# Kernel tuning notes

Measured on AMD Instinct MI355X. Metric: run time of the kernel, lower is better.

Reference implementation:

```python
import jax, jax.numpy as jnp
import numpy as np

B, M, N = 32, 16, 256        # problems, constraints, items
P = M * N                    # nodes per problem graph (4096)
NODES = B * P                # 131072
E = 2_097_152                # edges (avg degree 16)
F_IN = 16
H = 128                      # n_hidden[0..5], n_hidden[7]
H6 = 256                     # n_hidden[6]


def setup_inputs() -> dict:
    key = jax.random.key(0)
    ks = jax.random.split(key, 24)
    nrm = lambda k, shape: jax.random.normal(k, shape, jnp.float32) * 0.05
    inp = {}
    inp["G"] = jax.random.normal(ks[0], (NODES, F_IN), jnp.float32)
    inp["edge_index"] = jax.random.randint(ks[1], (2, E), 0, NODES)
    inp["edge_weight"] = jax.random.uniform(ks[2], (E,), jnp.float32)
    inp["edge_attribute"] = jax.random.normal(ks[3], (E, 1), jnp.float32)  # unused, kept for API parity
    inp["value_var_solutions"] = jax.random.randint(ks[4], (B, P), 0, 2).astype(jnp.int32)
    inp["item_values"] = jax.random.uniform(ks[5], (B, N), jnp.float32)
    # learned parameters
    inp["W_emb1"], inp["b_emb1"] = nrm(ks[6], (F_IN, H)), jnp.zeros((H,), jnp.float32)
    inp["W_emb2"], inp["b_emb2"] = nrm(ks[7], (H, H)), jnp.zeros((H,), jnp.float32)
    for i, t in enumerate(("c1", "c2")):  # GatedGraphConv(H, num_layers=2) x2
        inp[f"{t}_W"]  = nrm(ks[8 + 3 * i], (2, H, H))
        inp[f"{t}_wi"] = nrm(ks[9 + 3 * i], (3 * H, H))
        inp[f"{t}_wh"] = nrm(ks[10 + 3 * i], (3 * H, H))
        inp[f"{t}_bi"] = jnp.zeros((3 * H,), jnp.float32)
        inp[f"{t}_bh"] = jnp.zeros((3 * H,), jnp.float32)
    inp["W_g1"], inp["b_g1"] = nrm(ks[14], (H, H)), jnp.zeros((H,), jnp.float32)
    inp["W_g2"], inp["b_g2"] = nrm(ks[15], (H, H)), jnp.zeros((H,), jnp.float32)
    inp["W_l1"], inp["b_l1"] = nrm(ks[16], (2 * H, H6)), jnp.zeros((H6,), jnp.float32)
    inp["W_l2"], inp["b_l2"] = nrm(ks[17], (H6, H)), jnp.zeros((H,), jnp.float32)
    inp["W_l3"], inp["b_l3"] = nrm(ks[18], (H, 1)), jnp.zeros((1,), jnp.float32)
    return inp


def _gru_cell(m, h, wi, wh, bi, bh):
    # torch.nn.GRUCell with gate order (r, z, n)
    gi = m @ wi.T + bi
    gh = h @ wh.T + bh
    ir, iz, inn = jnp.split(gi, 3, axis=-1)
    hr, hz, hn = jnp.split(gh, 3, axis=-1)
    r = jax.nn.sigmoid(ir + hr)
    z = jax.nn.sigmoid(iz + hz)
    n = jnp.tanh(inn + r * hn)
    return (1.0 - z) * n + z * h


def _gated_graph_conv(x, src, dst, ew, W, wi, wh, bi, bh):
    # PyG GatedGraphConv: for each layer, m_i = sum_{j->i} ew * (x_j @ W_l); x = GRU(m, x)
    nnodes = x.shape[0]
    for l in range(W.shape[0]):
        msg = (x @ W[l])[src] * ew[:, None]          # [E, H]
        agg = jax.ops.segment_sum(msg, dst, num_segments=nnodes)
        x = _gru_cell(agg, x, wi, wh, bi, bh)
    return x


def reference(G, edge_index, edge_weight, edge_attribute, value_var_solutions, item_values,
              W_emb1, b_emb1, W_emb2, b_emb2,
              c1_W, c1_wi, c1_wh, c1_bi, c1_bh,
              c2_W, c2_wi, c2_wh, c2_bi, c2_bh,
              W_g1, b_g1, W_g2, b_g2,
              W_l1, b_l1, W_l2, b_l2, W_l3, b_l3):
    src, dst = edge_index[0], edge_index[1]
    x = jax.nn.relu(G @ W_emb1 + b_emb1)
    x = jax.nn.relu(x @ W_emb2 + b_emb2)
    x = jax.nn.relu(_gated_graph_conv(x, src, dst, edge_weight, c1_W, c1_wi, c1_wh, c1_bi, c1_bh))
    x = jax.nn.relu(_gated_graph_conv(x, src, dst, edge_weight, c2_W, c2_wi, c2_wh, c2_bi, c2_bh))
    x = jax.nn.relu(x @ W_g1 + b_g1)
    x = x @ W_g2 + b_g2                              # [NODES, H]
    # ragged per-graph mean pool + broadcast-concat (all graphs same size -> reshape)
    xg = x.reshape(B, P, H)
    ge = xg.mean(axis=1, keepdims=True)              # [B, 1, H] graph embedding
    u = jnp.concatenate([xg, jnp.broadcast_to(ge, xg.shape)], axis=-1)  # [B, P, 2H]
    u = jax.nn.relu(u @ W_l1 + b_l1)
    u = jax.nn.relu(u @ W_l2 + b_l2)
    u = (u @ W_l3 + b_l3)[..., 0]                    # [B, P]
    # bound: dx[j,i] = sol[0,i] - sol[j,i]; bound = u.dx + sum_i val[i]*sol[0,i]
    sol = value_var_solutions.reshape(B, M, N).astype(u.dtype)
    dx = sol[:, :1, :] - sol                         # [B, M, N]
    bounds = (jnp.einsum('bp,bp->b', u, dx.reshape(B, P))
              + jnp.einsum('bn,bn->b', item_values, sol[:, 0, :]))
    return bounds
```

## Files before the change

kernel.cpp:

```cpp
#include <hip/hip_runtime.h>

#define NODES   131072
#define EDGES   2097152
#define H       128
#define NB      32
#define PP      4096

typedef short bf16x8 __attribute__((ext_vector_type(8)));
typedef float f32x4  __attribute__((ext_vector_type(4)));
typedef float f32x2  __attribute__((ext_vector_type(2)));
typedef unsigned short u16;

#define RZE 65536
#define AIE 16384
#define AHE 16384
#define LYRE (RZE + AIE + AHE)

#define CAPP 18432

__global__ __launch_bounds__(128) void gnn_pinit(int* __restrict__ pcur) {
  pcur[threadIdx.x] = threadIdx.x * CAPP;
}

#define B1_BLOCKS 256
#define B1_TILES  4
__global__ __launch_bounds__(256) void gnn_bin1(const int* __restrict__ src, const int* __restrict__ dst,
                                                const float* __restrict__ ew, int* __restrict__ pcur,
                                                uint2* __restrict__ stage) {
  __shared__ int hist[128];
  __shared__ int pbase[128];
  const int tid = threadIdx.x;
  for (int t = 0; t < B1_TILES; ++t) {
    if (tid < 128) hist[tid] = 0;
    __syncthreads();
    const int ebase = blockIdx.x * (B1_TILES * 2048) + t * 2048;
    int parts[8], ranks[8];
    uint2 recs[8];
#pragma unroll
    for (int i = 0; i < 8; ++i) {
      int e = ebase + i * 256 + tid;
      int d = dst[e];
      int s = src[e];
      float w = ew[e];
      int wq = (int)fminf(w * 32768.f + 0.5f, 32767.f);
      parts[i] = d >> 10;
      recs[i].x = ((unsigned)s << 15) | (unsigned)wq;
      recs[i].y = (unsigned)d;
      ranks[i] = atomicAdd(&hist[parts[i]], 1);
    }
    __syncthreads();
    if (tid < 128) {
      int c = hist[tid];
      pbase[tid] = c ? atomicAdd(&pcur[tid], c) : 0;
    }
    __syncthreads();
#pragma unroll
    for (int i = 0; i < 8; ++i)
      stage[pbase[parts[i]] + ranks[i]] = recs[i];
    __syncthreads();
  }
}

__global__ __launch_bounds__(256) void gnn_bin2(const uint2* __restrict__ stage,
                                                const int* __restrict__ pcur,
                                                int* __restrict__ rowptr,
                                                unsigned* __restrict__ epack) {
  __shared__ int h[1024];
  __shared__ int ws[256];
  __shared__ int pc[128];
  __shared__ int gb_s;
  const int tid = threadIdx.x;
  const int p = blockIdx.x;
  const int node0 = p << 10;
  const int s0 = p * CAPP;
  const int cnt = pcur[p] - s0;
#pragma unroll
  for (int i = 0; i < 4; ++i) h[i * 256 + tid] = 0;
  if (tid < 128) pc[tid] = pcur[tid] - tid * CAPP;
  __syncthreads();
  for (int r = tid; r < cnt; r += 256)
    atomicAdd(&h[(int)stage[s0 + r].y - node0], 1);
  if (tid == 0) {
    int s = 0;
    for (int i = 0; i < p; ++i) s += pc[i];
    gb_s = s;
  }
  __syncthreads();
  const int gbase = gb_s;
  int a0 = h[tid * 4 + 0], a1 = h[tid * 4 + 1], a2 = h[tid * 4 + 2], a3 = h[tid * 4 + 3];
  int s1 = a0 + a1, s2 = s1 + a2, s3 = s2 + a3;
  ws[tid] = s3;
  __syncthreads();
  for (int o = 1; o < 256; o <<= 1) {
    int u = (tid >= o) ? ws[tid - o] : 0;
    __syncthreads();
    ws[tid] += u;
    __syncthreads();
  }
  int eb = gbase + (tid ? ws[tid - 1] : 0);
  int4 rp;
  rp.x = eb; rp.y = eb + a0; rp.z = eb + s1; rp.w = eb + s2;
  *(int4*)(rowptr + node0 + tid * 4) = rp;
  h[tid * 4 + 0] = rp.x; h[tid * 4 + 1] = rp.y; h[tid * 4 + 2] = rp.z; h[tid * 4 + 3] = rp.w;
  if (p == 127 && tid == 255) rowptr[NODES] = EDGES;
  __syncthreads();
  for (int r = tid; r < cnt; r += 256) {
    uint2 q = stage[s0 + r];
    int pos = atomicAdd(&h[(int)q.y - node0], 1);
    epack[pos] = q.x;
  }
}

__device__ __forceinline__ unsigned gnn_pack2bf(float a, float b) {
  union { float f; unsigned u; } x, y; x.f = a; y.f = b;
  unsigned ua = (x.u + 0x7FFFu + ((x.u >> 16) & 1u)) >> 16;
  unsigned ub = (y.u + 0x7FFFu + ((y.u >> 16) & 1u)) >> 16;
  return ua | (ub << 16);
}

__device__ __forceinline__ u16 gnn_f2bf(float a) {
  union { float f; unsigned u; } x; x.f = a;
  return (u16)((x.u + 0x7FFFu + ((x.u >> 16) & 1u)) >> 16);
}

__device__ __forceinline__ float gnn_bf2f(u16 h) {
  union { unsigned u; float f; } x; x.u = ((unsigned)h) << 16; return x.f;
}

__device__ __forceinline__ unsigned char gnn_f2fp8(float v) {
  return (unsigned char)(__builtin_amdgcn_cvt_pk_fp8_f32(v, v, 0, false) & 0xFF);
}

template<bool HI>
__device__ __forceinline__ unsigned gnn_bf2fp8pk(unsigned pv, unsigned old) {
  union { unsigned u; float f; } lo, hi;
  lo.u = pv << 16; hi.u = pv & 0xFFFF0000u;
  return __builtin_amdgcn_cvt_pk_fp8_f32(lo.f, hi.f, old, HI);
}

__device__ __forceinline__ float gnn_sig(float x)  { return 1.f / (1.f + __expf(-x)); }
__device__ __forceinline__ float gnn_tanh(float x) { return 1.f - 2.f / (1.f + __expf(2.f * x)); }

__global__ __launch_bounds__(256) void gnn_agg(const unsigned char* __restrict__ X8,
                                               const int* __restrict__ rowptr,
                                               const unsigned* __restrict__ epack,
                                               u16* __restrict__ T) {
  const int tid = threadIdx.x;
  const int wave = tid >> 6, lane = tid & 63;
  const int g = lane >> 4, s = lane & 15;
  const unsigned soff = (unsigned)(s << 3);
  const int node = blockIdx.x * 16 + wave * 4 + g;
  const int e1 = rowptr[node + 1];
  const int e0 = rowptr[node];
  float acc[8];
#pragma unroll
  for (int c = 0; c < 8; ++c) acc[c] = 0.f;

  for (int it = e0; __any(it < e1); it += 8) {
    unsigned qv[8];
#pragma unroll
    for (int j = 0; j < 8; ++j) {
      int t = it + j;
      t = t < e1 ? t : e1 - 1;
      t = t < 0 ? 0 : t;
      qv[j] = epack[t];
    }
    uint2 pv[8];
#pragma unroll
    for (int j = 0; j < 8; ++j)
      pv[j] = *(const uint2*)(X8 + ((((qv[j] >> 15) << 7)) | soff));
#pragma unroll
    for (int j = 0; j < 8; ++j) {
      float w = (it + j) < e1 ? (float)(qv[j] & 0x7FFFu) : 0.f;
      f32x2 f01 = __builtin_amdgcn_cvt_pk_f32_fp8(pv[j].x, false);
      f32x2 f23 = __builtin_amdgcn_cvt_pk_f32_fp8(pv[j].x, true);
      f32x2 f45 = __builtin_amdgcn_cvt_pk_f32_fp8(pv[j].y, false);
      f32x2 f67 = __builtin_amdgcn_cvt_pk_f32_fp8(pv[j].y, true);
      acc[0] = fmaf(w, f01.x, acc[0]);  acc[1] = fmaf(w, f01.y, acc[1]);
      acc[2] = fmaf(w, f23.x, acc[2]);  acc[3] = fmaf(w, f23.y, acc[3]);
      acc[4] = fmaf(w, f45.x, acc[4]);  acc[5] = fmaf(w, f45.y, acc[5]);
      acc[6] = fmaf(w, f67.x, acc[6]);  acc[7] = fmaf(w, f67.y, acc[7]);
    }
  }

  const float sc = 1.f / 32768.f;
  uint4 o;
  o.x = gnn_pack2bf(acc[0] * sc, acc[1] * sc);
  o.y = gnn_pack2bf(acc[2] * sc, acc[3] * sc);
  o.z = gnn_pack2bf(acc[4] * sc, acc[5] * sc);
  o.w = gnn_pack2bf(acc[6] * sc, acc[7] * sc);
  *(uint4*)(T + (long)node * H + s * 8) = o;
}

__global__ __launch_bounds__(384) void gnn_prep_wc_all(const float* __restrict__ c1W, const float* __restrict__ c1wi,
                                                       const float* __restrict__ c2W, const float* __restrict__ c2wi,
                                                       float* __restrict__ Wc) {
  __shared__ float wrow[128];
  int l = blockIdx.x >> 7, k = blockIdx.x & 127, j = threadIdx.x;
  const float* Wl = (l < 2 ? c1W : c2W) + (l & 1) * 128 * 128;
  const float* wi = l < 2 ? c1wi : c2wi;
  if (j < 128) wrow[j] = Wl[k * 128 + j];
  __syncthreads();
  float acc = 0.f;
  for (int m = 0; m < 128; ++m) acc = fmaf(wrow[m], wi[j * 128 + m], acc);
  Wc[(long)l * 49152 + k * 384 + j] = acc;
}

__global__ __launch_bounds__(384) void gnn_prep_whT(const float* __restrict__ wh1, const float* __restrict__ wh2,
                                                    float* __restrict__ whT) {
  int c = blockIdx.x >> 7, k = blockIdx.x & 127, j = threadIdx.x;
  const float* wh = c ? wh2 : wh1;
  whT[((long)c * 128 + k) * 384 + j] = wh[j * 128 + k];
}

template<int K>
__device__ __forceinline__ void gnn_stage_bf(const u16* __restrict__ A, long row0,
                                             u16* lds, int tid) {
  constexpr int CH = K / 8;
#pragma unroll
  for (int it = 0; it < (64 * CH) / 256; ++it) {
    int c = it * 256 + tid;
    int row = c / CH, ktq = c % CH;
    uint4 v = *(const uint4*)(A + (row0 + row) * K + ktq * 8);
    int slot = ktq * 64 + (row ^ (ktq & 7));
    *(uint4*)(lds + slot * 8) = v;
  }
}

template<int K>
__device__ __forceinline__ void gnn_stage32(const u16* __restrict__ A, long row0,
                                            u16* lds, int tid) {
  constexpr int CH = K / 8;
#pragma unroll
  for (int it = 0; it < (32 * CH) / 256; ++it) {
    int c = it * 256 + tid;
    int row = c / CH, ktq = c % CH;
    uint4 v = *(const uint4*)(A + (row0 + row) * K + ktq * 8);
    int slot = ktq * 32 + (row ^ (ktq & 7));
    *(uint4*)(lds + slot * 8) = v;
  }
}

__device__ __forceinline__ bf16x8 gnn_afrag(const u16* lds, int rt, int ktq, int l16) {
  int slot = ktq * 64 + ((rt * 16 + l16) ^ (ktq & 7));
  return *(const bf16x8*)(lds + slot * 8);
}

__device__ __forceinline__ bf16x8 gnn_afrag32(const u16* lds, int rt, int ktq, int l16) {
  int slot = ktq * 32 + ((rt * 16 + l16) ^ (ktq & 7));
  return *(const bf16x8*)(lds + slot * 8);
}

__device__ __forceinline__ bf16x8 gnn_bfrag(const u16* __restrict__ pk,
                                            int ct, int kt, int KT, int lane) {
  return *(const bf16x8*)(pk + (((long)(ct * KT + kt)) * 64 + lane) * 8);
}

__device__ __forceinline__ void gnn_lds_put(u16* lds, int row, int col, float v) {
  int kq = col >> 3, of = col & 7;
  lds[(kq * 64 + (row ^ (kq & 7))) * 8 + of] = gnn_f2bf(v);
}

__device__ __forceinline__ float gnn_lds_get(const u16* lds, int row, int col) {
  int kq = col >> 3, of = col & 7;
  return gnn_bf2f(lds[(kq * 64 + (row ^ (kq & 7))) * 8 + of]);
}

__device__ __forceinline__ float gnn_lds_get32(const u16* lds, int row, int col) {
  int kq = col >> 3, of = col & 7;
  return gnn_bf2f(lds[(kq * 32 + (row ^ (kq & 7))) * 8 + of]);
}

__device__ __forceinline__ void gnn_pack_body(const float* __restrict__ W0, const float* __restrict__ W1,
                                              int ksplit, int LD, int coff, int KT, int b, int lane,
                                              u16* __restrict__ dst) {
  int kt = b % KT, ct = b / KT;
  int col = ct * 16 + (lane & 15) + coff;
  int kb = kt * 32 + ((lane >> 4) & 3) * 8;
  u16 h[8];
#pragma unroll
  for (int j = 0; j < 8; ++j) {
    int k = kb + j;
    float v = (k < ksplit) ? W0[(long)k * LD + col] : W1[(long)(k - ksplit) * LD + col];
    h[j] = gnn_f2bf(v);
  }
  uint4 o;
  o.x = (unsigned)h[0] | ((unsigned)h[1] << 16);
  o.y = (unsigned)h[2] | ((unsigned)h[3] << 16);
  o.z = (unsigned)h[4] | ((unsigned)h[5] << 16);
  o.w = (unsigned)h[6] | ((unsigned)h[7] << 16);
  ((uint4*)dst)[(long)b * 64 + lane] = o;
}

__global__ __launch_bounds__(64) void gnn_pack_layers(const float* __restrict__ Wc, const float* __restrict__ whT,
                                                      u16* __restrict__ pk) {
  int l = blockIdx.x / 192, r = blockIdx.x % 192;
  int lane = threadIdx.x;
  const float* Wcl = Wc + (long)l * 49152;
  const float* whl = whT + (long)(l >> 1) * 49152;
  u16* base = pk + (long)l * LYRE;
  if (r < 128)      gnn_pack_body(Wcl, whl, 128, 384, 0,   8, r,       lane, base);
  else if (r < 160) gnn_pack_body(Wcl, Wcl, 128, 384, 256, 4, r - 128, lane, base + RZE);
  else              gnn_pack_body(whl, whl, 128, 384, 256, 4, r - 160, lane, base + RZE + AIE);
}

__global__ __launch_bounds__(64) void gnn_pack_misc(const float* __restrict__ We2, const float* __restrict__ Wg1,
                                                    const float* __restrict__ Wg2, const float* __restrict__ Wl1,
                                                    const float* __restrict__ Wl2, u16* __restrict__ pk) {
  int b = blockIdx.x, lane = threadIdx.x;
  u16* pe2 = pk + 4 * LYRE;
  if (b < 32)       gnn_pack_body(We2, We2, 128, 128, 0, 4, b,       lane, pe2);
  else if (b < 64)  gnn_pack_body(Wg1, Wg1, 128, 128, 0, 4, b - 32,  lane, pe2 + 16384);
  else if (b < 96)  gnn_pack_body(Wg2, Wg2, 128, 128, 0, 4, b - 64,  lane, pe2 + 32768);
  else if (b < 160) gnn_pack_body(Wl1, Wl1, 128, 256, 0, 4, b - 96,  lane, pe2 + 49152);
  else              gnn_pack_body(Wl2, Wl2, 256, 128, 0, 8, b - 160, lane, pe2 + 81920);
}

template<int K, int N, int ACT>
__global__ __launch_bounds__(256) void gnn_mgemm(const u16* __restrict__ A,
                                                 const u16* __restrict__ pk,
                                                 const float* __restrict__ bias,
                                                 u16* __restrict__ C,
                                                 unsigned char* __restrict__ C8) {
  constexpr int KT = K / 32;
  constexpr int CT = N / 64;
  __shared__ u16 As[64 * K];
  const int tid = threadIdx.x;
  const int lane = tid & 63, wave = tid >> 6;
  const int quad = lane >> 4, l16 = lane & 15;
  const long row0 = (long)blockIdx.x * 64;
  gnn_stage_bf<K>(A, row0, As, tid);
  __syncthreads();

  f32x4 zero4 = {0.f, 0.f, 0.f, 0.f};
  f32x4 acc[4][CT];
#pragma unroll
  for (int rt = 0; rt < 4; ++rt)
#pragma unroll
    for (int ct = 0; ct < CT; ++ct) acc[rt][ct] = zero4;

#pragma unroll
  for (int kt = 0; kt < KT; ++kt) {
    int ktq = kt * 4 + quad;
    bf16x8 af[4];
#pragma unroll
    for (int rt = 0; rt < 4; ++rt) af[rt] = gnn_afrag(As, rt, ktq, l16);
#pragma unroll
    for (int ct = 0; ct < CT; ++ct) {
      bf16x8 bf = gnn_bfrag(pk, wave * CT + ct, kt, KT, lane);
#pragma unroll
      for (int rt = 0; rt < 4; ++rt)
        acc[rt][ct] = __builtin_amdgcn_mfma_f32_16x16x32_bf16(af[rt], bf, acc[rt][ct], 0, 0, 0);
    }
  }

#pragma unroll
  for (int ct = 0; ct < CT; ++ct) {
    int col = (wave * CT + ct) * 16 + l16;
    float bv = bias[col];
#pragma unroll
    for (int rt = 0; rt < 4; ++rt) {
      long row = row0 + rt * 16 + quad * 4;
#pragma unroll
      for (int r = 0; r < 4; ++r) {
        float v = acc[rt][ct][r] + bv;
        if (ACT) v = fmaxf(v, 0.f);
        C[(row + r) * N + col] = gnn_f2bf(v);
        if (C8) C8[(row + r) * N + col] = gnn_f2fp8(v);
      }
    }
  }
}

#define OSTR 136

template<int RELU>
__global__ __launch_bounds__(256, 3) void gnn_mgru(const u16* __restrict__ T, const u16* __restrict__ X,
                                                   const u16* __restrict__ pkRZ,
                                                   const u16* __restrict__ pkAI,
                                                   const u16* __restrict__ pkAH,
                                                   const float* __restrict__ bi, const float* __restrict__ bh,
                                                   u16* __restrict__ Y,
                                                   unsigned char* __restrict__ Y8) {
  __shared__ u16 Ts[32 * OSTR];
  __shared__ u16 Xs[32 * 128];
  const int tid = threadIdx.x;
  const int lane = tid & 63, wave = tid >> 6;
  const int quad = lane >> 4, l16 = lane & 15;
  const long row0 = (long)blockIdx.x * 32;
  gnn_stage32<128>(T, row0, Ts, tid);
  gnn_stage32<128>(X, row0, Xs, tid);

  float brz[2], bzz[2], bin_[2], bhn[2];
#pragma unroll
  for (int c = 0; c < 2; ++c) {
    int col = (wave * 2 + c) * 16 + l16;
    brz[c]  = bi[col] + bh[col];
    bzz[c]  = bi[128 + col] + bh[128 + col];
    bin_[c] = bi[256 + col];
    bhn[c]  = bh[256 + col];
  }
  __syncthreads();

  f32x4 zero4 = {0.f, 0.f, 0.f, 0.f};
  f32x4 g1[2][2], g2[2][2];

#pragma unroll
  for (int rt = 0; rt < 2; ++rt)
#pragma unroll
    for (int c = 0; c < 2; ++c) g1[rt][c] = zero4;
#pragma unroll
  for (int kt = 0; kt < 4; ++kt) {
    int ktq = kt * 4 + quad;
    bf16x8 tf[2], xf[2];
#pragma unroll
    for (int rt = 0; rt < 2; ++rt) { tf[rt] = gnn_afrag32(Ts, rt, ktq, l16); xf[rt] = gnn_afrag32(Xs, rt, ktq, l16); }
#pragma unroll
    for (int c = 0; c < 2; ++c) {
      int ct = wave * 2 + c;
      bf16x8 bRT = gnn_bfrag(pkRZ, ct, kt,     8, lane);
      bf16x8 bRX = gnn_bfrag(pkRZ, ct, kt + 4, 8, lane);
#pragma unroll
      for (int rt = 0; rt < 2; ++rt) {
        g1[rt][c] = __builtin_amdgcn_mfma_f32_16x16x32_bf16(tf[rt], bRT, g1[rt][c], 0, 0, 0);
        g1[rt][c] = __builtin_amdgcn_mfma_f32_16x16x32_bf16(xf[rt], bRX, g1[rt][c], 0, 0, 0);
      }
    }
  }
#pragma unroll
  for (int rt = 0; rt < 2; ++rt)
#pragma unroll
    for (int c = 0; c < 2; ++c)
#pragma unroll
      for (int r = 0; r < 4; ++r)
        g1[rt][c][r] = gnn_sig(g1[rt][c][r] + brz[c]);

#pragma unroll
  for (int rt = 0; rt < 2; ++rt)
#pragma unroll
    for (int c = 0; c < 2; ++c) g2[rt][c] = zero4;
#pragma unroll
  for (int kt = 0; kt < 4; ++kt) {
    int ktq = kt * 4 + quad;
    bf16x8 xf[2];
#pragma unroll
    for (int rt = 0; rt < 2; ++rt) xf[rt] = gnn_afrag32(Xs, rt, ktq, l16);
#pragma unroll
    for (int c = 0; c < 2; ++c) {
      bf16x8 bAH = gnn_bfrag(pkAH, wave * 2 + c, kt, 4, lane);
#pragma unroll
      for (int rt = 0; rt < 2; ++rt)
        g2[rt][c] = __builtin_amdgcn_mfma_f32_16x16x32_bf16(xf[rt], bAH, g2[rt][c], 0, 0, 0);
    }
  }
#pragma unroll
  for (int rt = 0; rt < 2; ++rt)
#pragma unroll
    for (int c = 0; c < 2; ++c)
#pragma unroll
      for (int r = 0; r < 4; ++r)
        g1[rt][c][r] = g1[rt][c][r] * (g2[rt][c][r] + bhn[c]);

#pragma unroll
  for (int rt = 0; rt < 2; ++rt)
#pragma unroll
    for (int c = 0; c < 2; ++c) g2[rt][c] = zero4;
#pragma unroll
  for (int kt = 0; kt < 4; ++kt) {
    int ktq = kt * 4 + quad;
    bf16x8 tf[2];
#pragma unroll
    for (int rt = 0; rt < 2; ++rt) tf[rt] = gnn_afrag32(Ts, rt, ktq, l16);
#pragma unroll
    for (int c = 0; c < 2; ++c) {
      bf16x8 bAI = gnn_bfrag(pkAI, wave * 2 + c, kt, 4, lane);
#pragma unroll
      for (int rt = 0; rt < 2; ++rt)
        g2[rt][c] = __builtin_amdgcn_mfma_f32_16x16x32_bf16(tf[rt], bAI, g2[rt][c], 0, 0, 0);
    }
  }
#pragma unroll
  for (int rt = 0; rt < 2; ++rt)
#pragma unroll
    for (int c = 0; c < 2; ++c)
#pragma unroll
      for (int r = 0; r < 4; ++r)
        g1[rt][c][r] = gnn_tanh(g2[rt][c][r] + bin_[c] + g1[rt][c][r]);

#pragma unroll
  for (int rt = 0; rt < 2; ++rt)
#pragma unroll
    for (int c = 0; c < 2; ++c) g2[rt][c] = zero4;
#pragma unroll
  for (int kt = 0; kt < 4; ++kt) {
    int ktq = kt * 4 + quad;
    bf16x8 tf[2], xf[2];
#pragma unroll
    for (int rt = 0; rt < 2; ++rt) { tf[rt] = gnn_afrag32(Ts, rt, ktq, l16); xf[rt] = gnn_afrag32(Xs, rt, ktq, l16); }
#pragma unroll
    for (int c = 0; c < 2; ++c) {
      int ct = wave * 2 + c;
      bf16x8 bZT = gnn_bfrag(pkRZ, 8 + ct, kt,     8, lane);
      bf16x8 bZX = gnn_bfrag(pkRZ, 8 + ct, kt + 4, 8, lane);
#pragma unroll
      for (int rt = 0; rt < 2; ++rt) {
        g2[rt][c] = __builtin_amdgcn_mfma_f32_16x16x32_bf16(tf[rt], bZT, g2[rt][c], 0, 0, 0);
        g2[rt][c] = __builtin_amdgcn_mfma_f32_16x16x32_bf16(xf[rt], bZX, g2[rt][c], 0, 0, 0);
      }
    }
  }

  float yv[2][2][4];
#pragma unroll
  for (int rt = 0; rt < 2; ++rt)
#pragma unroll
    for (int c = 0; c < 2; ++c) {
      int col = (wave * 2 + c) * 16 + l16;
      int rowl = rt * 16 + quad * 4;
#pragma unroll
      for (int r = 0; r < 4; ++r) {
        float z = gnn_sig(g2[rt][c][r] + bzz[c]);
        float h = gnn_lds_get32(Xs, rowl + r, col);
        float v = (1.f - z) * g1[rt][c][r] + z * h;
        if (RELU) v = fmaxf(v, 0.f);
        yv[rt][c][r] = v;
      }
    }
  __syncthreads();
#pragma unroll
  for (int rt = 0; rt < 2; ++rt)
#pragma unroll
    for (int c = 0; c < 2; ++c) {
      int col = (wave * 2 + c) * 16 + l16;
      int rowl = rt * 16 + quad * 4;
#pragma unroll
      for (int r = 0; r < 4; ++r)
        Ts[(rowl + r) * OSTR + col] = gnn_f2bf(yv[rt][c][r]);
    }
  __syncthreads();
  {
    const int orow = tid >> 3;
    const int oc = (tid & 7) * 16;
    const u16* src = Ts + orow * OSTR + oc;
    uint4 a = *(const uint4*)(src);
    uint4 b = *(const uint4*)(src + 8);
    u16* yd = Y + (row0 + orow) * H + oc;
    *(uint4*)(yd) = a;
    *(uint4*)(yd + 8) = b;
    if (Y8) {
      uint4 o8;
      o8.x = gnn_bf2fp8pk<true>(a.y, gnn_bf2fp8pk<false>(a.x, 0));
      o8.y = gnn_bf2fp8pk<true>(a.w, gnn_bf2fp8pk<false>(a.z, 0));
      o8.z = gnn_bf2fp8pk<true>(b.y, gnn_bf2fp8pk<false>(b.x, 0));
      o8.w = gnn_bf2fp8pk<true>(b.w, gnn_bf2fp8pk<false>(b.z, 0));
      *(uint4*)(Y8 + (row0 + orow) * H + oc) = o8;
    }
  }
}

__global__ __launch_bounds__(256) void gnn_g1g2(const u16* __restrict__ A,
                                                const u16* __restrict__ pk1, const float* __restrict__ b1,
                                                const u16* __restrict__ pk2, const float* __restrict__ b2,
                                                u16* __restrict__ C, float* __restrict__ ge) {
  __shared__ u16 As[64 * 128];
  __shared__ u16 Ys[64 * 128];
  const int tid = threadIdx.x;
  const int lane = tid & 63, wave = tid >> 6;
  const int quad = lane >> 4, l16 = lane & 15;
  const long row0 = (long)blockIdx.x * 64;
  gnn_stage_bf<128>(A, row0, As, tid);
  __syncthreads();

  f32x4 zero4 = {0.f, 0.f, 0.f, 0.f};
  f32x4 acc[4][2];
#pragma unroll
  for (int rt = 0; rt < 4; ++rt)
#pragma unroll
    for (int ct = 0; ct < 2; ++ct) acc[rt][ct] = zero4;
#pragma unroll
  for (int kt = 0; kt < 4; ++kt) {
    int ktq = kt * 4 + quad;
    bf16x8 af[4];
#pragma unroll
    for (int rt = 0; rt < 4; ++rt) af[rt] = gnn_afrag(As, rt, ktq, l16);
#pragma unroll
    for (int ct = 0; ct < 2; ++ct) {
      bf16x8 bf = gnn_bfrag(pk1, wave * 2 + ct, kt, 4, lane);
#pragma unroll
      for (int rt = 0; rt < 4; ++rt)
        acc[rt][ct] = __builtin_amdgcn_mfma_f32_16x16x32_bf16(af[rt], bf, acc[rt][ct], 0, 0, 0);
    }
  }
#pragma unroll
  for (int ct = 0; ct < 2; ++ct) {
    int col = (wave * 2 + ct) * 16 + l16;
    float bv = b1[col];
#pragma unroll
    for (int rt = 0; rt < 4; ++rt) {
      int rowl = rt * 16 + quad * 4;
#pragma unroll
      for (int r = 0; r < 4; ++r)
        gnn_lds_put(Ys, rowl + r, col, fmaxf(acc[rt][ct][r] + bv, 0.f));
    }
  }
  __syncthreads();

  f32x4 acc2[4][2];
#pragma unroll
  for (int rt = 0; rt < 4; ++rt)
#pragma unroll
    for (int ct = 0; ct < 2; ++ct) acc2[rt][ct] = zero4;
#pragma unroll
  for (int kt = 0; kt < 4; ++kt) {
    int ktq = kt * 4 + quad;
    bf16x8 af[4];
#pragma unroll
    for (int rt = 0; rt < 4; ++rt) af[rt] = gnn_afrag(Ys, rt, ktq, l16);
#pragma unroll
    for (int ct = 0; ct < 2; ++ct) {
      bf16x8 bf = gnn_bfrag(pk2, wave * 2 + ct, kt, 4, lane);
#pragma unroll
      for (int rt = 0; rt < 4; ++rt)
        acc2[rt][ct] = __builtin_amdgcn_mfma_f32_16x16x32_bf16(af[rt], bf, acc2[rt][ct], 0, 0, 0);
    }
  }
  float psum[2];
#pragma unroll
  for (int ct = 0; ct < 2; ++ct) {
    int col = (wave * 2 + ct) * 16 + l16;
    float bv = b2[col];
    float cs = 0.f;
#pragma unroll
    for (int rt = 0; rt < 4; ++rt) {
      long row = row0 + rt * 16 + quad * 4;
#pragma unroll
      for (int r = 0; r < 4; ++r) {
        float v = acc2[rt][ct][r] + bv;
        cs += v;
        C[(row + r) * H + col] = gnn_f2bf(v);
      }
    }
    psum[ct] = cs;
  }
  const int b = (int)(row0 >> 12);
#pragma unroll
  for (int ct = 0; ct < 2; ++ct) {
    float v = psum[ct];
    v += __shfl_xor(v, 16);
    v += __shfl_xor(v, 32);
    if (quad == 0) {
      int col = (wave * 2 + ct) * 16 + l16;
      atomicAdd(&ge[b * H + col], v);
    }
  }
}

__global__ __launch_bounds__(256) void gnn_l1l2(const u16* __restrict__ A,
                                                const u16* __restrict__ pk1, const float* __restrict__ gb,
                                                const u16* __restrict__ pk2, const float* __restrict__ b2,
                                                u16* __restrict__ C) {
  __shared__ u16 As[64 * 128];
  __shared__ u16 Us[64 * 256];
  const int tid = threadIdx.x;
  const int lane = tid & 63, wave = tid >> 6;
  const int quad = lane >> 4, l16 = lane & 15;
  const long row0 = (long)blockIdx.x * 64;
  gnn_stage_bf<128>(A, row0, As, tid);
  __syncthreads();

  f32x4 zero4 = {0.f, 0.f, 0.f, 0.f};
  {
    f32x4 acc[4][4];
#pragma unroll
    for (int rt = 0; rt < 4; ++rt)
#pragma unroll
      for (int ct = 0; ct < 4; ++ct) acc[rt][ct] = zero4;
#pragma unroll
    for (int kt = 0; kt < 4; ++kt) {
      int ktq = kt * 4 + quad;
      bf16x8 af[4];
#pragma unroll
      for (int rt = 0; rt < 4; ++rt) af[rt] = gnn_afrag(As, rt, ktq, l16);
#pragma unroll
      for (int ct = 0; ct < 4; ++ct) {
        bf16x8 bf = gnn_bfrag(pk1, wave * 4 + ct, kt, 4, lane);
#pragma unroll
        for (int rt = 0; rt < 4; ++rt)
          acc[rt][ct] = __builtin_amdgcn_mfma_f32_16x16x32_bf16(af[rt], bf, acc[rt][ct], 0, 0, 0);
      }
    }
    const float* bp = gb + (row0 >> 12) * 256;
#pragma unroll
    for (int ct = 0; ct < 4; ++ct) {
      int col = (wave * 4 + ct) * 16 + l16;
      float bv = bp[col];
#pragma unroll
      for (int rt = 0; rt < 4; ++rt) {
        int rowl = rt * 16 + quad * 4;
#pragma unroll
        for (int r = 0; r < 4; ++r)
          gnn_lds_put(Us, rowl + r, col, fmaxf(acc[rt][ct][r] + bv, 0.f));
      }
    }
  }
  __syncthreads();

  f32x4 acc2[4][2];
#pragma unroll
  for (int rt = 0; rt < 4; ++rt)
#pragma unroll
    for (int ct = 0; ct < 2; ++ct) acc2[rt][ct] = zero4;
#pragma unroll
  for (int kt = 0; kt < 8; ++kt) {
    int ktq = kt * 4 + quad;
    bf16x8 af[4];
#pragma unroll
    for (int rt = 0; rt < 4; ++rt) af[rt] = gnn_afrag(Us, rt, ktq, l16);
#pragma unroll
    for (int ct = 0; ct < 2; ++ct) {
      bf16x8 bf = gnn_bfrag(pk2, wave * 2 + ct, kt, 8, lane);
#pragma unroll
      for (int rt = 0; rt < 4; ++rt)
        acc2[rt][ct] = __builtin_amdgcn_mfma_f32_16x16x32_bf16(af[rt], bf, acc2[rt][ct], 0, 0, 0);
    }
  }
#pragma unroll
  for (int ct = 0; ct < 2; ++ct) {
    int col = (wave * 2 + ct) * 16 + l16;
    float bv = b2[col];
#pragma unroll
    for (int rt = 0; rt < 4; ++rt) {
      long row = row0 + rt * 16 + quad * 4;
#pragma unroll
      for (int r = 0; r < 4; ++r)
        C[(row + r) * H + col] = gnn_f2bf(fmaxf(acc2[rt][ct][r] + bv, 0.f));
    }
  }
}

#define GFMA(i, av) \
  acc[(i)*4+0] = fmaf((av), wv.x, acc[(i)*4+0]); \
  acc[(i)*4+1] = fmaf((av), wv.y, acc[(i)*4+1]); \
  acc[(i)*4+2] = fmaf((av), wv.z, acc[(i)*4+2]); \
  acc[(i)*4+3] = fmaf((av), wv.w, acc[(i)*4+3]);

__global__ __launch_bounds__(256) void gnn_gemm16(const float* __restrict__ A, const float* __restrict__ W,
                                                  const float* __restrict__ bias, u16* __restrict__ C,
                                                  int OUT) {
  const int K = 16;
  __shared__ float AsT[16][68];
  __shared__ float Ws[16][68];
  const int tid = threadIdx.x;
  const int tx = tid & 15, ty = tid >> 4;
  const long row0 = (long)blockIdx.y * 64;
  const int col0 = blockIdx.x * 64;
  const int lr  = tid >> 2;
  const int lk4 = (tid & 3) * 4;
  const int wk  = tid >> 4;
  const int wj4 = (tid & 15) * 4;
  float acc[16];
#pragma unroll
  for (int i = 0; i < 16; ++i) acc[i] = 0.f;

  {
    float4 a = *(const float4*)(A + (row0 + lr) * K + lk4);
    float4 w = *(const float4*)(W + (long)wk * OUT + col0 + wj4);
    AsT[lk4 + 0][lr] = a.x; AsT[lk4 + 1][lr] = a.y; AsT[lk4 + 2][lr] = a.z; AsT[lk4 + 3][lr] = a.w;
    *(float4*)(&Ws[wk][wj4]) = w;
    __syncthreads();
#pragma unroll
    for (int k = 0; k < 16; ++k) {
      float4 av = *(const float4*)(&AsT[k][ty * 4]);
      float4 wv = *(const float4*)(&Ws[k][tx * 4]);
      GFMA(0, av.x) GFMA(1, av.y) GFMA(2, av.z) GFMA(3, av.w)
    }
  }
#pragma unroll
  for (int i = 0; i < 4; ++i) {
    long row = row0 + ty * 4 + i;
    int j = col0 + tx * 4;
    float4 o;
    o.x = fmaxf(acc[i * 4 + 0] + bias[j + 0], 0.f);
    o.y = fmaxf(acc[i * 4 + 1] + bias[j + 1], 0.f);
    o.z = fmaxf(acc[i * 4 + 2] + bias[j + 2], 0.f);
    o.w = fmaxf(acc[i * 4 + 3] + bias[j + 3], 0.f);
    uint2 st;
    st.x = gnn_pack2bf(o.x, o.y);
    st.y = gnn_pack2bf(o.z, o.w);
    *(uint2*)(C + row * OUT + j) = st;
  }
}
#undef GFMA

__global__ __launch_bounds__(256) void gnn_gbias(const float* __restrict__ ge, const float* __restrict__ Wl1b,
                                                 const float* __restrict__ bl1, float* __restrict__ gb) {
  __shared__ float g[128];
  int b = blockIdx.x, t = threadIdx.x;
  if (t < 128) g[t] = ge[b * H + t] * (1.f / 4096.f);
  __syncthreads();
  float acc = bl1[t];
  for (int k = 0; k < 128; ++k) acc = fmaf(g[k], Wl1b[k * 256 + t], acc);
  gb[b * 256 + t] = acc;
}

__global__ __launch_bounds__(256) void gnn_item(const float* __restrict__ iv, const int* __restrict__ vvs,
                                                float* __restrict__ out) {
  __shared__ float s[256];
  int b = blockIdx.x, t = threadIdx.x;
  float v = iv[b * 256 + t] * (float)vvs[(long)b * PP + t];
  s[t] = v; __syncthreads();
  for (int off = 128; off > 0; off >>= 1) {
    if (t < off) s[t] += s[t + off];
    __syncthreads();
  }
  if (t == 0) out[b] = s[0];
}

__global__ __launch_bounds__(256) void gnn_bound(const u16* __restrict__ U2, const float* __restrict__ wl3,
                                                 const float* __restrict__ bl3, const int* __restrict__ vvs,
                                                 float* __restrict__ out) {
  int tid = threadIdx.x;
  int wave = tid >> 6, lane = tid & 63;
  int b = blockIdx.x >> 6;
  long node0 = (long)blockIdx.x * 64 + wave * 16;
  float w0 = wl3[lane * 2], w1 = wl3[lane * 2 + 1];
  float bl = bl3[0];
  float acc = 0.f;
  for (int i = 0; i < 16; ++i) {
    long node = node0 + i;
    unsigned pv = *(const unsigned*)(U2 + node * H + lane * 2);
    union { unsigned u; float f; } lo, hi;
    lo.u = pv << 16; hi.u = pv & 0xFFFF0000u;
    float p = lo.f * w0 + hi.f * w1;
#pragma unroll
    for (int off = 32; off > 0; off >>= 1) p += __shfl_down(p, off);
    if (lane == 0) {
      int pp = (int)(node & (PP - 1));
      int m = pp >> 8, n = pp & 255;
      if (m != 0) {
        float dx = (float)(vvs[((long)b << 12) + n] - vvs[((long)b << 12) + pp]);
        acc += (p + bl) * dx;
      }
    }
  }
  __shared__ float s[4];
  if (lane == 0) s[wave] = acc;
  __syncthreads();
  if (tid == 0) atomicAdd(&out[b], s[0] + s[1] + s[2] + s[3]);
}

extern "C" void kernel_launch(void* const* d_in, const int* in_sizes, int n_in,
                              void* d_out, int out_size, void* d_ws, size_t ws_size,
                              hipStream_t stream) {
  const float* G      = (const float*)d_in[0];
  const int*   ei     = (const int*)d_in[1];
  const int*   esrc   = ei;
  const int*   edst   = ei + EDGES;
  const float* ew     = (const float*)d_in[2];
  const int*   vvs    = (const int*)d_in[4];
  const float* iv     = (const float*)d_in[5];
  const float* W_emb1 = (const float*)d_in[6];
  const float* b_emb1 = (const float*)d_in[7];
  const float* W_emb2 = (const float*)d_in[8];
  const float* b_emb2 = (const float*)d_in[9];
  const float* c1_W   = (const float*)d_in[10];
  const float* c1_wi  = (const float*)d_in[11];
  const float* c1_wh  = (const float*)d_in[12];
  const float* c1_bi  = (const float*)d_in[13];
  const float* c1_bh  = (const float*)d_in[14];
  const float* c2_W   = (const float*)d_in[15];
  const float* c2_wi  = (const float*)d_in[16];
  const float* c2_wh  = (const float*)d_in[17];
  const float* c2_bi  = (const float*)d_in[18];
  const float* c2_bh  = (const float*)d_in[19];
  const float* W_g1   = (const float*)d_in[20];
  const float* b_g1   = (const float*)d_in[21];
  const float* W_g2   = (const float*)d_in[22];
  const float* b_g2   = (const float*)d_in[23];
  const float* W_l1   = (const float*)d_in[24];
  const float* b_l1   = (const float*)d_in[25];
  const float* W_l2   = (const float*)d_in[26];
  const float* b_l2   = (const float*)d_in[27];
  const float* W_l3   = (const float*)d_in[28];
  const float* b_l3   = (const float*)d_in[29];
  float* out = (float*)d_out;
  (void)in_sizes; (void)n_in; (void)out_size; (void)ws_size;

  char* wsb = (char*)d_ws;
  size_t off = 0;
  auto carve = [&](size_t bytes) -> char* {
    char* p = wsb + off;
    off += (bytes + 255) & ~(size_t)255;
    return p;
  };
  u16*   xa     = (u16*)carve(sizeof(u16) * (size_t)NODES * H);
  u16*   xc     = (u16*)carve(sizeof(u16) * (size_t)NODES * H);
  u16*   tb     = (u16*)carve(sizeof(u16) * (size_t)NODES * H);
  float* Wc     = (float*)carve(sizeof(float) * 4 * H * 384);
  float* whT    = (float*)carve(sizeof(float) * 2 * H * 384);
  u16*   pk     = (u16*)carve(sizeof(u16) * 507904);
  int*   rowptr = (int*)carve(sizeof(int) * (NODES + 1));
  int*   pcur   = (int*)carve(sizeof(int) * 128);
  uint2* stage  = (uint2*)carve(sizeof(uint2) * (size_t)128 * CAPP);
  unsigned* epack = (unsigned*)carve(sizeof(unsigned) * EDGES);
  float* ge     = (float*)carve(sizeof(float) * NB * H);
  float* gb     = (float*)carve(sizeof(float) * NB * 256);

  unsigned char* X8 = (unsigned char*)stage;

  u16* pkRZ[4]; u16* pkAI[4]; u16* pkAH[4];
  for (int l = 0; l < 4; ++l) {
    pkRZ[l] = pk + (long)l * LYRE;
    pkAI[l] = pk + (long)l * LYRE + RZE;
    pkAH[l] = pk + (long)l * LYRE + RZE + AIE;
  }
  u16* pe2 = pk + 4 * LYRE;
  u16* pg1 = pe2 + 16384;
  u16* pg2 = pe2 + 32768;
  u16* pl1 = pe2 + 49152;
  u16* pl2 = pe2 + 81920;

  hipMemsetAsync(ge, 0, sizeof(float) * NB * H, stream);
  gnn_pinit<<<1, 128, 0, stream>>>(pcur);
  gnn_bin1<<<B1_BLOCKS, 256, 0, stream>>>(esrc, edst, ew, pcur, stage);
  gnn_bin2<<<128, 256, 0, stream>>>(stage, pcur, rowptr, epack);

  gnn_prep_wc_all<<<512, 384, 0, stream>>>(c1_W, c1_wi, c2_W, c2_wi, Wc);
  gnn_prep_whT<<<256, 384, 0, stream>>>(c1_wh, c2_wh, whT);
  gnn_pack_layers<<<768, 64, 0, stream>>>(Wc, whT, pk);
  gnn_pack_misc<<<224, 64, 0, stream>>>(W_emb2, W_g1, W_g2, W_l1, W_l2, pk);

  gnn_gemm16<<<dim3(2, NODES / 64), 256, 0, stream>>>(G, W_emb1, b_emb1, xa, 128);
  gnn_mgemm<128, 128, 1><<<NODES / 64, 256, 0, stream>>>(xa, pe2, b_emb2, xc, X8);

  gnn_agg<<<NODES / 16, 256, 0, stream>>>(X8, rowptr, epack, tb);
  gnn_mgru<0><<<NODES / 32, 256, 0, stream>>>(tb, xc, pkRZ[0], pkAI[0], pkAH[0], c1_bi, c1_bh, xa, X8);
  gnn_agg<<<NODES / 16, 256, 0, stream>>>(X8, rowptr, epack, tb);
  gnn_mgru<1><<<NODES / 32, 256, 0, stream>>>(tb, xa, pkRZ[1], pkAI[1], pkAH[1], c1_bi, c1_bh, xc, X8);

  gnn_agg<<<NODES / 16, 256, 0, stream>>>(X8, rowptr, epack, tb);
  gnn_mgru<0><<<NODES / 32, 256, 0, stream>>>(tb, xc, pkRZ[2], pkAI[2], pkAH[2], c2_bi, c2_bh, xa, X8);
  gnn_agg<<<NODES / 16, 256, 0, stream>>>(X8, rowptr, epack, tb);
  gnn_mgru<1><<<NODES / 32, 256, 0, stream>>>(tb, xa, pkRZ[3], pkAI[3], pkAH[3], c2_bi, c2_bh, xc, nullptr);

  gnn_g1g2<<<NODES / 64, 256, 0, stream>>>(xc, pg1, b_g1, pg2, b_g2, tb, ge);

  gnn_gbias<<<NB, 256, 0, stream>>>(ge, W_l1 + 128 * 256, b_l1, gb);

  gnn_l1l2<<<NODES / 64, 256, 0, stream>>>(tb, pl1, gb, pl2, b_l2, xa);

  gnn_item<<<NB, 256, 0, stream>>>(iv, vvs, out);
  gnn_bound<<<NODES / 64, 256, 0, stream>>>(xa, W_l3, b_l3, vvs, out);
}
```

Baseline: 754.7 us.

## Fuse embedding GEMMs into one kernel and merge weight-prep launches

Fuses the first embedding layer (16->128 FP32 GEMM with ReLU) into the second MFMA embedding GEMM. The intermediate activations now stay in LDS, so the bf16 round trip through global memory and one launch are removed. It also merges the two weight-prep kernels into one launch and the two weight-pack kernels into another, cutting launch count. The fused kernel uses more LDS per block, which could lower occupancy.

```diff
diff --git a/kernel.cpp b/kernel.cpp
--- a/kernel.cpp
+++ b/kernel.cpp
@@ -192,25 +192,26 @@
   *(uint4*)(T + (long)node * H + s * 8) = o;
 }
 
-__global__ __launch_bounds__(384) void gnn_prep_wc_all(const float* __restrict__ c1W, const float* __restrict__ c1wi,
-                                                       const float* __restrict__ c2W, const float* __restrict__ c2wi,
-                                                       float* __restrict__ Wc) {
-  __shared__ float wrow[128];
-  int l = blockIdx.x >> 7, k = blockIdx.x & 127, j = threadIdx.x;
-  const float* Wl = (l < 2 ? c1W : c2W) + (l & 1) * 128 * 128;
-  const float* wi = l < 2 ? c1wi : c2wi;
-  if (j < 128) wrow[j] = Wl[k * 128 + j];
-  __syncthreads();
-  float acc = 0.f;
-  for (int m = 0; m < 128; ++m) acc = fmaf(wrow[m], wi[j * 128 + m], acc);
-  Wc[(long)l * 49152 + k * 384 + j] = acc;
-}
-
-__global__ __launch_bounds__(384) void gnn_prep_whT(const float* __restrict__ wh1, const float* __restrict__ wh2,
-                                                    float* __restrict__ whT) {
-  int c = blockIdx.x >> 7, k = blockIdx.x & 127, j = threadIdx.x;
-  const float* wh = c ? wh2 : wh1;
-  whT[((long)c * 128 + k) * 384 + j] = wh[j * 128 + k];
+__global__ __launch_bounds__(384) void gnn_prep(const float* __restrict__ c1W, const float* __restrict__ c1wi,
+                                                const float* __restrict__ c2W, const float* __restrict__ c2wi,
+                                                const float* __restrict__ wh1, const float* __restrict__ wh2,
+                                                float* __restrict__ Wc, float* __restrict__ whT) {
+  if (blockIdx.x < 512) {
+    __shared__ float wrow[128];
+    int l = blockIdx.x >> 7, k = blockIdx.x & 127, j = threadIdx.x;
+    const float* Wl = (l < 2 ? c1W : c2W) + (l & 1) * 128 * 128;
+    const float* wi = l < 2 ? c1wi : c2wi;
+    if (j < 128) wrow[j] = Wl[k * 128 + j];
+    __syncthreads();
+    float acc = 0.f;
+    for (int m = 0; m < 128; ++m) acc = fmaf(wrow[m], wi[j * 128 + m], acc);
+    Wc[(long)l * 49152 + k * 384 + j] = acc;
+  } else {
+    int bb = blockIdx.x - 512;
+    int c = bb >> 7, k = bb & 127, j = threadIdx.x;
+    const float* wh = c ? wh2 : wh1;
+    whT[((long)c * 128 + k) * 384 + j] = wh[j * 128 + k];
+  }
 }
 
 template<int K>
@@ -292,81 +293,122 @@
   ((uint4*)dst)[(long)b * 64 + lane] = o;
 }
 
-__global__ __launch_bounds__(64) void gnn_pack_layers(const float* __restrict__ Wc, const float* __restrict__ whT,
-                                                      u16* __restrict__ pk) {
-  int l = blockIdx.x / 192, r = blockIdx.x % 192;
+__global__ __launch_bounds__(64) void gnn_pack(const float* __restrict__ Wc, const float* __restrict__ whT,
+                                               const float* __restrict__ We2, const float* __restrict__ Wg1,
+                                               const float* __restrict__ Wg2, const float* __restrict__ Wl1,
+                                               const float* __restrict__ Wl2, u16* __restrict__ pk) {
   int lane = threadIdx.x;
-  const float* Wcl = Wc + (long)l * 49152;
-  const float* whl = whT + (long)(l >> 1) * 49152;
-  u16* base = pk + (long)l * LYRE;
-  if (r < 128)      gnn_pack_body(Wcl, whl, 128, 384, 0,   8, r,       lane, base);
-  else if (r < 160) gnn_pack_body(Wcl, Wcl, 128, 384, 256, 4, r - 128, lane, base + RZE);
-  else              gnn_pack_body(whl, whl, 128, 384, 256, 4, r - 160, lane, base + RZE + AIE);
-}
-
-__global__ __launch_bounds__(64) void gnn_pack_misc(const float* __restrict__ We2, const float* __restrict__ Wg1,
-                                                    const float* __restrict__ Wg2, const float* __restrict__ Wl1,
-                                                    const float* __restrict__ Wl2, u16* __restrict__ pk) {
-  int b = blockIdx.x, lane = threadIdx.x;
-  u16* pe2 = pk + 4 * LYRE;
-  if (b < 32)       gnn_pack_body(We2, We2, 128, 128, 0, 4, b,       lane, pe2);
-  else if (b < 64)  gnn_pack_body(Wg1, Wg1, 128, 128, 0, 4, b - 32,  lane, pe2 + 16384);
-  else if (b < 96)  gnn_pack_body(Wg2, Wg2, 128, 128, 0, 4, b - 64,  lane, pe2 + 32768);
-  else if (b < 160) gnn_pack_body(Wl1, Wl1, 128, 256, 0, 4, b - 96,  lane, pe2 + 49152);
-  else              gnn_pack_body(Wl2, Wl2, 256, 128, 0, 8, b - 160, lane, pe2 + 81920);
-}
-
-template<int K, int N, int ACT>
-__global__ __launch_bounds__(256) void gnn_mgemm(const u16* __restrict__ A,
-                                                 const u16* __restrict__ pk,
-                                                 const float* __restrict__ bias,
-                                                 u16* __restrict__ C,
-                                                 unsigned char* __restrict__ C8) {
-  constexpr int KT = K / 32;
-  constexpr int CT = N / 64;
-  __shared__ u16 As[64 * K];
+  if (blockIdx.x < 768) {
+    int l = blockIdx.x / 192, r = blockIdx.x % 192;
+    const float* Wcl = Wc + (long)l * 49152;
+    const float* whl = whT + (long)(l >> 1) * 49152;
+    u16* base = pk + (long)l * LYRE;
+    if (r < 128)      gnn_pack_body(Wcl, whl, 128, 384, 0,   8, r,       lane, base);
+    else if (r < 160) gnn_pack_body(Wcl, Wcl, 128, 384, 256, 4, r - 128, lane, base + RZE);
+    else              gnn_pack_body(whl, whl, 128, 384, 256, 4, r - 160, lane, base + RZE + AIE);
+  } else {
+    int b = blockIdx.x - 768;
+    u16* pe2 = pk + 4 * LYRE;
+    if (b < 32)       gnn_pack_body(We2, We2, 128, 128, 0, 4, b,       lane, pe2);
+    else if (b < 64)  gnn_pack_body(Wg1, Wg1, 128, 128, 0, 4, b - 32,  lane, pe2 + 16384);
+    else if (b < 96)  gnn_pack_body(Wg2, Wg2, 128, 128, 0, 4, b - 64,  lane, pe2 + 32768);
+    else if (b < 160) gnn_pack_body(Wl1, Wl1, 128, 256, 0, 4, b - 96,  lane, pe2 + 49152);
+    else              gnn_pack_body(Wl2, Wl2, 256, 128, 0, 8, b - 160, lane, pe2 + 81920);
+  }
+}
+
+__global__ __launch_bounds__(256) void gnn_emb(const float* __restrict__ G, const float* __restrict__ W1,
+                                               const float* __restrict__ b1,
+                                               const u16* __restrict__ pk2, const float* __restrict__ b2,
+                                               u16* __restrict__ C, unsigned char* __restrict__ C8) {
+  __shared__ u16 As[64 * 128];
+  __shared__ float AsT[16][68];
+  __shared__ float Ws[16][132];
   const int tid = threadIdx.x;
   const int lane = tid & 63, wave = tid >> 6;
   const int quad = lane >> 4, l16 = lane & 15;
   const long row0 = (long)blockIdx.x * 64;
-  gnn_stage_bf<K>(A, row0, As, tid);
+
+  {
+    const int lr  = tid >> 2;
+    const int lk4 = (tid & 3) * 4;
+    const int wk  = tid >> 4;
+    const int wj4 = (tid & 15) * 4;
+    float4 a = *(const float4*)(G + (row0 + lr) * 16 + lk4);
+    AsT[lk4 + 0][lr] = a.x; AsT[lk4 + 1][lr] = a.y; AsT[lk4 + 2][lr] = a.z; AsT[lk4 + 3][lr] = a.w;
+    float4 w0 = *(const float4*)(W1 + (long)wk * 128 + wj4);
+    float4 w1 = *(const float4*)(W1 + (long)wk * 128 + 64 + wj4);
+    *(float4*)(&Ws[wk][wj4]) = w0;
+    *(float4*)(&Ws[wk][64 + wj4]) = w1;
+    __syncthreads();
+
+    const int tx = tid & 15, ty = tid >> 4;
+    float acc0[16], acc1[16];
+#pragma unroll
+    for (int i = 0; i < 16; ++i) { acc0[i] = 0.f; acc1[i] = 0.f; }
+#pragma unroll
+    for (int k = 0; k < 16; ++k) {
+      float4 av  = *(const float4*)(&AsT[k][ty * 4]);
+      float4 wv0 = *(const float4*)(&Ws[k][tx * 4]);
+      float4 wv1 = *(const float4*)(&Ws[k][64 + tx * 4]);
+#pragma unroll
+      for (int i = 0; i < 4; ++i) {
+        float av_i = (i == 0) ? av.x : (i == 1) ? av.y : (i == 2) ? av.z : av.w;
+        acc0[i * 4 + 0] = fmaf(av_i, wv0.x, acc0[i * 4 + 0]);
+        acc0[i * 4 + 1] = fmaf(av_i, wv0.y, acc0[i * 4 + 1]);
+        acc0[i * 4 + 2] = fmaf(av_i, wv0.z, acc0[i * 4 + 2]);
+        acc0[i * 4 + 3] = fmaf(av_i, wv0.w, acc0[i * 4 + 3]);
+        acc1[i * 4 + 0] = fmaf(av_i, wv1.x, acc1[i * 4 + 0]);
+        acc1[i * 4 + 1] = fmaf(av_i, wv1.y, acc1[i * 4 + 1]);
+        acc1[i * 4 + 2] = fmaf(av_i, wv1.z, acc1[i * 4 + 2]);
+        acc1[i * 4 + 3] = fmaf(av_i, wv1.w, acc1[i * 4 + 3]);
+      }
+    }
+#pragma unroll
+    for (int i = 0; i < 4; ++i) {
+      int row = ty * 4 + i;
+#pragma unroll
+      for (int j = 0; j < 4; ++j) {
+        int c0 = tx * 4 + j;
+        gnn_lds_put(As, row, c0,      fmaxf(acc0[i * 4 + j] + b1[c0], 0.f));
+        gnn_lds_put(As, row, c0 + 64, fmaxf(acc1[i * 4 + j] + b1[c0 + 64], 0.f));
+      }
+    }
+  }
   __syncthreads();
 
   f32x4 zero4 = {0.f, 0.f, 0.f, 0.f};
-  f32x4 acc[4][CT];
+  f32x4 acc[4][2];
 #pragma unroll
   for (int rt = 0; rt < 4; ++rt)
 #pragma unroll
-    for (int ct = 0; ct < CT; ++ct) acc[rt][ct] = zero4;
-
-#pragma unroll
-  for (int kt = 0; kt < KT; ++kt) {
+    for (int ct = 0; ct < 2; ++ct) acc[rt][ct] = zero4;
+#pragma unroll
+  for (int kt = 0; kt < 4; ++kt) {
     int ktq = kt * 4 + quad;
     bf16x8 af[4];
 #pragma unroll
     for (int rt = 0; rt < 4; ++rt) af[rt] = gnn_afrag(As, rt, ktq, l16);
 #pragma unroll
-    for (int ct = 0; ct < CT; ++ct) {
-      bf16x8 bf = gnn_bfrag(pk, wave * CT + ct, kt, KT, lane);
+    for (int ct = 0; ct < 2; ++ct) {
+      bf16x8 bf = gnn_bfrag(pk2, wave * 2 + ct, kt, 4, lane);
 #pragma unroll
       for (int rt = 0; rt < 4; ++rt)
         acc[rt][ct] = __builtin_amdgcn_mfma_f32_16x16x32_bf16(af[rt], bf, acc[rt][ct], 0, 0, 0);
     }
   }
-
-#pragma unroll
-  for (int ct = 0; ct < CT; ++ct) {
-    int col = (wave * CT + ct) * 16 + l16;
-    float bv = bias[col];
+#pragma unroll
+  for (int ct = 0; ct < 2; ++ct) {
+    int col = (wave * 2 + ct) * 16 + l16;
+    float bv = b2[col];
 #pragma unroll
     for (int rt = 0; rt < 4; ++rt) {
       long row = row0 + rt * 16 + quad * 4;
 #pragma unroll
       for (int r = 0; r < 4; ++r) {
-        float v = acc[rt][ct][r] + bv;
-        if (ACT) v = fmaxf(v, 0.f);
-        C[(row + r) * N + col] = gnn_f2bf(v);
-        if (C8) C8[(row + r) * N + col] = gnn_f2fp8(v);
+        float v = fmaxf(acc[rt][ct][r] + bv, 0.f);
+        C[(row + r) * H + col] = gnn_f2bf(v);
+        C8[(row + r) * H + col] = gnn_f2fp8(v);
       }
     }
   }
@@ -737,60 +779,6 @@
     }
   }
 }
-
-#define GFMA(i, av) \
-  acc[(i)*4+0] = fmaf((av), wv.x, acc[(i)*4+0]); \
-  acc[(i)*4+1] = fmaf((av), wv.y, acc[(i)*4+1]); \
-  acc[(i)*4+2] = fmaf((av), wv.z, acc[(i)*4+2]); \
-  acc[(i)*4+3] = fmaf((av), wv.w, acc[(i)*4+3]);
-
-__global__ __launch_bounds__(256) void gnn_gemm16(const float* __restrict__ A, const float* __restrict__ W,
-                                                  const float* __restrict__ bias, u16* __restrict__ C,
-                                                  int OUT) {
-  const int K = 16;
-  __shared__ float AsT[16][68];
-  __shared__ float Ws[16][68];
-  const int tid = threadIdx.x;
-  const int tx = tid & 15, ty = tid >> 4;
-  const long row0 = (long)blockIdx.y * 64;
-  const int col0 = blockIdx.x * 64;
-  const int lr  = tid >> 2;
-  const int lk4 = (tid & 3) * 4;
-  const int wk  = tid >> 4;
-  const int wj4 = (tid & 15) * 4;
-  float acc[16];
-#pragma unroll
-  for (int i = 0; i < 16; ++i) acc[i] = 0.f;
-
-  {
-    float4 a = *(const float4*)(A + (row0 + lr) * K + lk4);
-    float4 w = *(const float4*)(W + (long)wk * OUT + col0 + wj4);
-    AsT[lk4 + 0][lr] = a.x; AsT[lk4 + 1][lr] = a.y; AsT[lk4 + 2][lr] = a.z; AsT[lk4 + 3][lr] = a.w;
-    *(float4*)(&Ws[wk][wj4]) = w;
-    __syncthreads();
-#pragma unroll
-    for (int k = 0; k < 16; ++k) {
-      float4 av = *(const float4*)(&AsT[k][ty * 4]);
-      float4 wv = *(const float4*)(&Ws[k][tx * 4]);
-      GFMA(0, av.x) GFMA(1, av.y) GFMA(2, av.z) GFMA(3, av.w)
-    }
-  }
-#pragma unroll
-  for (int i = 0; i < 4; ++i) {
-    long row = row0 + ty * 4 + i;
-    int j = col0 + tx * 4;
-    float4 o;
-    o.x = fmaxf(acc[i * 4 + 0] + bias[j + 0], 0.f);
-    o.y = fmaxf(acc[i * 4 + 1] + bias[j + 1], 0.f);
-    o.z = fmaxf(acc[i * 4 + 2] + bias[j + 2], 0.f);
-    o.w = fmaxf(acc[i * 4 + 3] + bias[j + 3], 0.f);
-    uint2 st;
-    st.x = gnn_pack2bf(o.x, o.y);
-    st.y = gnn_pack2bf(o.z, o.w);
-    *(uint2*)(C + row * OUT + j) = st;
-  }
-}
-#undef GFMA
 
 __global__ __launch_bounds__(256) void gnn_gbias(const float* __restrict__ ge, const float* __restrict__ Wl1b,
                                                  const float* __restrict__ bl1, float* __restrict__ gb) {
@@ -925,13 +913,10 @@
   gnn_bin1<<<B1_BLOCKS, 256, 0, stream>>>(esrc, edst, ew, pcur, stage);
   gnn_bin2<<<128, 256, 0, stream>>>(stage, pcur, rowptr, epack);
 
-  gnn_prep_wc_all<<<512, 384, 0, stream>>>(c1_W, c1_wi, c2_W, c2_wi, Wc);
-  gnn_prep_whT<<<256, 384, 0, stream>>>(c1_wh, c2_wh, whT);
-  gnn_pack_layers<<<768, 64, 0, stream>>>(Wc, whT, pk);
-  gnn_pack_misc<<<224, 64, 0, stream>>>(W_emb2, W_g1, W_g2, W_l1, W_l2, pk);
-
-  gnn_gemm16<<<dim3(2, NODES / 64), 256, 0, stream>>>(G, W_emb1, b_emb1, xa, 128);
-  gnn_mgemm<128, 128, 1><<<NODES / 64, 256, 0, stream>>>(xa, pe2, b_emb2, xc, X8);
+  gnn_prep<<<768, 384, 0, stream>>>(c1_W, c1_wi, c2_W, c2_wi, c1_wh, c2_wh, Wc, whT);
+  gnn_pack<<<992, 64, 0, stream>>>(Wc, whT, W_emb2, W_g1, W_g2, W_l1, W_l2, pk);
+
+  gnn_emb<<<NODES / 64, 256, 0, stream>>>(G, W_emb1, b_emb1, pe2, b_emb2, xc, X8);
 
   gnn_agg<<<NODES / 16, 256, 0, stream>>>(X8, rowptr, epack, tb);
   gnn_mgru<0><<<NODES / 32, 256, 0, stream>>>(tb, xc, pkRZ[0], pkAI[0], pkAH[0], c1_bi, c1_bh, xa, X8);
```

Measured after the change: 705.5 us. 6.5% less time.
